# Kernel tuning notes

Measured on AMD Instinct MI355X. Metric: run time of the kernel, lower is better.

The kernel has to match this reference:

```python
import jax, jax.numpy as jnp
import numpy as np

B, L, H, NL = 2048, 32, 512, 64  # batch rows, max children, w_dim, num_labels
EPS = 1e-5


def _layernorm(x, g, b):
    mu = jnp.mean(x, axis=-1, keepdims=True)
    var = jnp.mean((x - mu) ** 2, axis=-1, keepdims=True)
    return (x - mu) * jax.lax.rsqrt(var + EPS) * g + b


def _lstm(x, Wih, Whh, bih, bhh):
    # x: [B, L, D] -> h: [B, L, H]; PyTorch gate order i, f, g, o
    Bs, Ls, _ = x.shape
    Hh = Whh.shape[1]
    xg = jnp.einsum('bld,gd->blg', x, Wih) + bih + bhh  # [B, L, 4H]

    def step(carry, xg_t):
        h, c = carry
        gates = xg_t + h @ Whh.T
        i, f, g, o = jnp.split(gates, 4, axis=-1)
        c = jax.nn.sigmoid(f) * c + jax.nn.sigmoid(i) * jnp.tanh(g)
        h = jax.nn.sigmoid(o) * jnp.tanh(c)
        return (h, c), h

    init = (jnp.zeros((Bs, Hh), x.dtype), jnp.zeros((Bs, Hh), x.dtype))
    _, hs = jax.lax.scan(step, init, jnp.swapaxes(xg, 0, 1))
    return jnp.swapaxes(hs, 0, 1)


def setup_inputs() -> dict:
    key = jax.random.key(0)
    ks = jax.random.split(key, 20)
    n = lambda k, shape, s=0.05: (jax.random.normal(k, shape, jnp.float32) * s)
    return {
        'children': n(ks[0], (B, L, H), 1.0),
        'ch_lengths': jax.random.randint(ks[1], (B,), 1, L + 1),
        'nt': n(ks[2], (B, H), 1.0),
        'nt_id': jax.random.randint(ks[3], (B,), 0, NL),
        'stack_state': n(ks[4], (B, H), 1.0),
        'Wih_f': n(ks[5], (4 * H, H)), 'Whh_f': n(ks[6], (4 * H, H)),
        'bih_f': jnp.zeros(4 * H, jnp.float32), 'bhh_f': jnp.zeros(4 * H, jnp.float32),
        'Wih_b': n(ks[7], (4 * H, H)), 'Whh_b': n(ks[8], (4 * H, H)),
        'bih_b': jnp.zeros(4 * H, jnp.float32), 'bhh_b': jnp.zeros(4 * H, jnp.float32),
        'V': n(ks[9], (2 * H, 2 * H)),
        'nt_emb': n(ks[10], (NL, H), 1.0),
        'nt_emb2': n(ks[11], (NL, 2 * H), 1.0),
        'ln1_g': jnp.ones(2 * H, jnp.float32), 'ln1_b': jnp.zeros(2 * H, jnp.float32),
        'ln2_g': jnp.ones(2 * H, jnp.float32), 'ln2_b': jnp.zeros(2 * H, jnp.float32),
        'gate_W': n(ks[12], (2 * H, 4 * H)), 'gate_b': jnp.zeros(2 * H, jnp.float32),
        'out_W': n(ks[13], (H, 2 * H)), 'out_b': jnp.zeros(H, jnp.float32),
    }


def reference(children, ch_lengths, nt, nt_id, stack_state,
              Wih_f, Whh_f, bih_f, bhh_f, Wih_b, Whh_b, bih_b, bhh_b,
              V, nt_emb, nt_emb2, ln1_g, ln1_b, ln2_g, ln2_b,
              gate_W, gate_b, out_W, out_b):
    t = jnp.arange(L)
    valid = (t[None, :] < ch_lengths[:, None])  # [B, L]
    mask = valid[:, :, None].astype(children.dtype)

    # forward direction (padded positions cannot affect earlier outputs)
    h_f = _lstm(children, Wih_f, Whh_f, bih_f, bhh_f) * mask

    # backward direction: emulate packed sequence by per-row reversal over true length
    rev_idx = jnp.clip(ch_lengths[:, None] - 1 - t[None, :], 0, L - 1)  # [B, L]
    x_rev = jnp.take_along_axis(children, rev_idx[:, :, None], axis=1) * mask
    h_b_rev = _lstm(x_rev, Wih_b, Whh_b, bih_b, bhh_b)
    h_b = jnp.take_along_axis(h_b_rev, rev_idx[:, :, None], axis=1) * mask

    h = jnp.concatenate([h_f, h_b], axis=-1)  # [B, L, 2H]

    rhs = jnp.concatenate([nt_emb[nt_id], stack_state], axis=1)  # [B, 2H]
    logit = jnp.einsum('ble,de,bd->bl', h, V, rhs)  # (V h) . rhs
    logit = jnp.where(valid, logit, -jnp.inf)
    attn = jax.nn.softmax(logit, axis=-1)  # [B, L]

    weighted_child = jnp.einsum('ble,bl->be', h, attn)  # [B, 2H]
    weighted_child = _layernorm(weighted_child, ln2_g, ln2_b)

    nt2 = _layernorm(nt_emb2[nt_id], ln1_g, ln1_b)  # [B, 2H]
    gate_in = jnp.concatenate([nt2, weighted_child], axis=-1)  # [B, 4H]
    g = jax.nn.sigmoid(gate_in @ gate_W.T + gate_b)  # [B, 2H]
    c = g * nt2 + (1.0 - g) * weighted_child
    out = jax.nn.relu(c @ out_W.T + out_b)  # [B, H]
    return (out, attn, g)
```

## Files before the change

kernel.cpp:

```cpp
#include <hip/hip_runtime.h>

#define B_ 2048
#define L_ 32
#define H_ 512
#define H2 1024
#define H4 2048

typedef _Float16 half8 __attribute__((ext_vector_type(8)));
typedef _Float16 half4v __attribute__((ext_vector_type(4)));
typedef float f32x4 __attribute__((ext_vector_type(4)));

__device__ __forceinline__ float sigm(float x) { return 1.f / (1.f + __expf(-x)); }
__device__ __forceinline__ float tanh_f(float x) {
  float ax = fabsf(x);
  float e = __expf(2.f * ax);
  float t = 1.f - 2.f / (e + 1.f);
  return x < 0.f ? -t : t;
}
__device__ __forceinline__ float wave_sum(float v) {
#pragma unroll
  for (int o = 32; o; o >>= 1) v += __shfl_xor(v, o);
  return v;
}

__device__ __forceinline__ void gload_lds16(const _Float16* g, _Float16* l) {
  __builtin_amdgcn_global_load_lds((const __attribute__((address_space(1))) void*)g,
                                   (__attribute__((address_space(3))) void*)l, 16, 0, 0);
}

__global__ __launch_bounds__(256, 2) void gemm_bt(
    const _Float16* __restrict__ A, int lda,
    const _Float16* __restrict__ Bmat, int ldb,
    float* __restrict__ C, int ldc, int K)
{
  __shared__ _Float16 As[2][128 * 64];
  __shared__ _Float16 Bs[2][128 * 64];
  const int tid = threadIdx.x;
  const int lane = tid & 63;
  const int w = tid >> 6;
  const int n0 = blockIdx.x * 128;
  const int m0 = blockIdx.y * 128;

  const int srow = lane >> 3;
  const int kcs = ((lane & 7) ^ srow) << 3;

  f32x4 acc[4][4] = {};
  const int wm = (w >> 1) * 64;
  const int wn = (w & 1) * 64;
  const int fr = lane & 15;

  const int nkt = K >> 6;
  auto stage = [&](int buf, int kt) {
    const int k0 = kt << 6;
#pragma unroll
    for (int i = 0; i < 4; ++i) {
      const int R0 = w * 32 + i * 8;
      gload_lds16(A + (size_t)(m0 + R0 + srow) * lda + (k0 + kcs), &As[buf][R0 * 64]);
      gload_lds16(Bmat + (size_t)(n0 + R0 + srow) * ldb + (k0 + kcs), &Bs[buf][R0 * 64]);
    }
  };

  stage(0, 0);
  __syncthreads();
  int cur = 0;
  for (int kt = 0; kt < nkt; ++kt) {
    if (kt + 1 < nkt) stage(cur ^ 1, kt + 1);
    const char* Ab = (const char*)&As[cur][0];
    const char* Bb = (const char*)&Bs[cur][0];
#pragma unroll
    for (int kk = 0; kk < 2; ++kk) {
      const int so = (((kk << 2) + (lane >> 4)) ^ (fr & 7)) << 4;
      half8 af[4], bf[4];
#pragma unroll
      for (int m = 0; m < 4; ++m) af[m] = *(const half8*)(Ab + (wm + m * 16 + fr) * 128 + so);
#pragma unroll
      for (int n = 0; n < 4; ++n) bf[n] = *(const half8*)(Bb + (wn + n * 16 + fr) * 128 + so);
#pragma unroll
      for (int m = 0; m < 4; ++m)
#pragma unroll
        for (int n = 0; n < 4; ++n)
          acc[m][n] = __builtin_amdgcn_mfma_f32_16x16x32_f16(af[m], bf[n], acc[m][n], 0, 0, 0);
    }
    __syncthreads();
    cur ^= 1;
  }

  const int r0 = (lane >> 4) * 4;
#pragma unroll
  for (int m = 0; m < 4; ++m)
#pragma unroll
    for (int n = 0; n < 4; ++n)
#pragma unroll
      for (int r = 0; r < 4; ++r) {
        const int row = m0 + wm + m * 16 + r0 + r;
        const int col = n0 + wn + n * 16 + fr;
        C[(size_t)row * ldc + col] = acc[m][n][r];
      }
}

__global__ __launch_bounds__(256, 2) void gemm_lstm(
    const _Float16* __restrict__ Wpack,
    const float* __restrict__ bpack,
    const _Float16* __restrict__ chH,
    _Float16* __restrict__ hstate,
    float* __restrict__ cstate,
    _Float16* __restrict__ h_all,
    const int* __restrict__ perm,
    const int* __restrict__ lens_sorted,
    int step)
{
  const int lin = blockIdx.x;
  const int xcd = lin & 7;
  const int g8 = lin >> 3;
  const int dir = xcd >> 2;
  const int quad = xcd & 3;
  const int mt = (quad >> 1) * 8 + (g8 >> 3);
  const int nt = (quad & 1) * 8 + (g8 & 7);
  const int m0 = mt * 128;
  const int n0 = nt * 128;
  if (lens_sorted[m0] <= step) return;

  __shared__ _Float16 As[2][128 * 64];
  __shared__ _Float16 Bs[2][128 * 64];
  const int tid = threadIdx.x;
  const int lane = tid & 63;
  const int w = tid >> 6;

  const int srow = lane >> 3;
  const int kcs = ((lane & 7) ^ srow) << 3;

  const _Float16* xsrc[4];
  int posr[4];
#pragma unroll
  for (int i = 0; i < 4; ++i) {
    const int pos = m0 + w * 32 + i * 8 + srow;
    const int b = perm[pos];
    int idx;
    if (dir == 0) idx = step;
    else { const int t = lens_sorted[pos] - 1 - step; idx = t < 0 ? 0 : (t > 31 ? 31 : t); }
    xsrc[i] = chH + ((size_t)b * L_ + idx) * H_ + kcs;
    posr[i] = pos;
  }
  const _Float16* Wb = Wpack + (size_t)dir * H4 * H2;
  const _Float16* hs = hstate + (size_t)dir * B_ * H_;

  f32x4 acc[4][4] = {};
  const int wm = (w >> 1) * 64;
  const int wn = (w & 1) * 64;
  const int fr = lane & 15;

  auto stage = [&](int buf, int kt) {
    const int k0 = kt << 6;
#pragma unroll
    for (int i = 0; i < 4; ++i) {
      const int R0 = w * 32 + i * 8;
      const _Float16* sA = (k0 < 512) ? (xsrc[i] + k0)
                                      : (hs + (size_t)posr[i] * H_ + (k0 - 512) + kcs);
      gload_lds16(sA, &As[buf][R0 * 64]);
      gload_lds16(Wb + (size_t)(n0 + R0 + srow) * H2 + k0 + kcs, &Bs[buf][R0 * 64]);
    }
  };

  stage(0, 0);
  __syncthreads();
  int cur = 0;
  for (int kt = 0; kt < 16; ++kt) {
    if (kt + 1 < 16) stage(cur ^ 1, kt + 1);
    const char* Ab = (const char*)&As[cur][0];
    const char* Bb = (const char*)&Bs[cur][0];
#pragma unroll
    for (int kk = 0; kk < 2; ++kk) {
      const int so = (((kk << 2) + (lane >> 4)) ^ (fr & 7)) << 4;
      half8 af[4], bf[4];
#pragma unroll
      for (int m = 0; m < 4; ++m) af[m] = *(const half8*)(Ab + (wm + m * 16 + fr) * 128 + so);
#pragma unroll
      for (int n = 0; n < 4; ++n) bf[n] = *(const half8*)(Bb + (wn + n * 16 + fr) * 128 + so);
#pragma unroll
      for (int m = 0; m < 4; ++m)
#pragma unroll
        for (int n = 0; n < 4; ++n)
          acc[m][n] = __builtin_amdgcn_mfma_f32_16x16x32_f16(af[m], bf[n], acc[m][n], 0, 0, 0);
    }
    __syncthreads();
    cur ^= 1;
  }

  const int r0 = (lane >> 4) * 4;
  const int j = ((n0 + wn) >> 6) * 16 + fr;
  const float bi = bpack[dir * H4 + n0 + wn + 0 * 16 + fr];
  const float bf_ = bpack[dir * H4 + n0 + wn + 1 * 16 + fr];
  const float bg = bpack[dir * H4 + n0 + wn + 2 * 16 + fr];
  const float bo = bpack[dir * H4 + n0 + wn + 3 * 16 + fr];
  float* cs = cstate + (size_t)dir * B_ * H_;
  _Float16* hsw = hstate + (size_t)dir * B_ * H_;

#pragma unroll
  for (int m = 0; m < 4; ++m)
#pragma unroll
    for (int r = 0; r < 4; ++r) {
      const int pos = m0 + wm + m * 16 + r0 + r;
      const float zi = acc[m][0][r] + bi;
      const float zf = acc[m][1][r] + bf_;
      const float zg = acc[m][2][r] + bg;
      const float zo = acc[m][3][r] + bo;
      const size_t ci = (size_t)pos * H_ + j;
      const float cn = sigm(zf) * cs[ci] + sigm(zi) * tanh_f(zg);
      const float h = sigm(zo) * tanh_f(cn);
      cs[ci] = cn;
      hsw[ci] = (_Float16)h;
      const int len = lens_sorted[pos];
      if (step < len) {
        const int b = perm[pos];
        const int t = (dir == 0) ? step : (len - 1 - step);
        h_all[((size_t)b * L_ + t) * H2 + dir * 512 + j] = (_Float16)h;
      }
    }
}

__global__ void cast_half_k(const float* __restrict__ s, _Float16* __restrict__ d, int n) {
  const int i = (blockIdx.x * 256 + threadIdx.x) * 4;
  if (i >= n) return;
  const float4 v = *(const float4*)(s + i);
  half4v h;
  h[0] = (_Float16)v.x; h[1] = (_Float16)v.y; h[2] = (_Float16)v.z; h[3] = (_Float16)v.w;
  *(half4v*)(d + i) = h;
}

__global__ void pack_wcat(const float* __restrict__ Wih_f, const float* __restrict__ Whh_f,
                          const float* __restrict__ Wih_b, const float* __restrict__ Whh_b,
                          _Float16* __restrict__ Wcat) {
  const int idx = blockIdx.x * 256 + threadIdx.x;
  const int k = idx & 511;
  const int c = (idx >> 9) & 2047;
  const int dir = idx >> 20;
  const int g = (c >> 4) & 3;
  const int j = ((c >> 6) << 4) + (c & 15);
  const int n_orig = g * 512 + j;
  const float* Wih = dir ? Wih_b : Wih_f;
  const float* Whh = dir ? Whh_b : Whh_f;
  _Float16* row = Wcat + ((size_t)dir * H4 + c) * H2;
  row[k] = (_Float16)Wih[(size_t)n_orig * H_ + k];
  row[512 + k] = (_Float16)Whh[(size_t)n_orig * H_ + k];
}

__global__ void pack_bias(const float* __restrict__ bih_f, const float* __restrict__ bhh_f,
                          const float* __restrict__ bih_b, const float* __restrict__ bhh_b,
                          float* __restrict__ biascat) {
  const int idx = blockIdx.x * 256 + threadIdx.x;
  const int dir = idx >> 11;
  const int c = idx & 2047;
  const int g = (c >> 4) & 3;
  const int j = ((c >> 6) << 4) + (c & 15);
  const int n = g * 512 + j;
  biascat[idx] = dir ? (bih_b[n] + bhh_b[n]) : (bih_f[n] + bhh_f[n]);
}

__global__ void transpose_v(const float* __restrict__ V, _Float16* __restrict__ Vt) {
  const int idx = blockIdx.x * 256 + threadIdx.x;
  const int d = idx >> 10;
  const int e = idx & 1023;
  Vt[(size_t)e * H2 + d] = (_Float16)V[idx];
}

__global__ void build_rhs(const float* __restrict__ nt_emb, const int* __restrict__ nt_id,
                          const float* __restrict__ stack_state, _Float16* __restrict__ rhs_h) {
  const int idx = blockIdx.x * 256 + threadIdx.x;
  const int b = idx >> 10;
  const int d = idx & 1023;
  const float v = (d < 512) ? nt_emb[(size_t)nt_id[b] * H_ + d]
                            : stack_state[(size_t)b * H_ + (d - 512)];
  rhs_h[idx] = (_Float16)v;
}

__global__ void sort1_k(const int* __restrict__ lens, int* __restrict__ offs, int* __restrict__ cursor) {
  __shared__ int cnt[33];
  const int tid = threadIdx.x;
  if (tid < 33) cnt[tid] = 0;
  __syncthreads();
  for (int i = tid; i < B_; i += 256) atomicAdd(&cnt[lens[i]], 1);
  __syncthreads();
  if (tid == 0) {
    int acc = 0;
    for (int l = 32; l >= 1; --l) { offs[l] = acc; acc += cnt[l]; }
  }
  if (tid < 33) cursor[tid] = 0;
}

__global__ void sort2_k(const int* __restrict__ lens, const int* __restrict__ offs,
                        int* __restrict__ cursor, int* __restrict__ perm,
                        int* __restrict__ lens_sorted) {
  const int b = blockIdx.x * 256 + threadIdx.x;
  const int len = lens[b];
  const int pos = offs[len] + atomicAdd(&cursor[len], 1);
  perm[pos] = b;
  lens_sorted[pos] = len;
}

__global__ void marker_k(float* out) { out[threadIdx.x] = 12345.0f; }

__global__ __launch_bounds__(256) void attn_kernel(
    const _Float16* __restrict__ h_all, const float* __restrict__ u,
    const int* __restrict__ lens,
    const float* __restrict__ g2, const float* __restrict__ b2,
    float* __restrict__ attn_out, float* __restrict__ wc_f, _Float16* __restrict__ gin_h) {
  __shared__ float u_s[H2];
  __shared__ float logit_s[L_];
  __shared__ float attn_s[L_];
  __shared__ float red_s[8];
  const int b = blockIdx.x;
  const int tid = threadIdx.x;
  const int lane = tid & 63;
  const int w = tid >> 6;
#pragma unroll
  for (int r = 0; r < 4; ++r) u_s[tid + r * 256] = u[(size_t)b * H2 + tid + r * 256];
  __syncthreads();
  const _Float16* hb = h_all + (size_t)b * L_ * H2;
  const int len = lens[b];
#pragma unroll
  for (int li = 0; li < 8; ++li) {
    const int l = w * 8 + li;
    float p = 0.f;
    if (l < len) {
      const _Float16* hr = hb + (size_t)l * H2;
#pragma unroll
      for (int j = 0; j < 16; ++j) {
        const int e = lane + 64 * j;
        p += (float)hr[e] * u_s[e];
      }
      p = wave_sum(p);
    }
    if (lane == 0) logit_s[l] = p;
  }
  __syncthreads();
  if (w == 0) {
    const int l = lane;
    float v = (l < len) ? logit_s[l] : -1e30f;
    float m = v;
#pragma unroll
    for (int o = 32; o; o >>= 1) m = fmaxf(m, __shfl_xor(m, o));
    const float e = (l < len) ? __expf(v - m) : 0.f;
    float s = e;
#pragma unroll
    for (int o = 32; o; o >>= 1) s += __shfl_xor(s, o);
    const float a = e / s;
    if (l < L_) { attn_s[l] = a; attn_out[(size_t)b * L_ + l] = a; }
  }
  __syncthreads();
  float wcv[4] = {0.f, 0.f, 0.f, 0.f};
  for (int l = 0; l < len; ++l) {
    const float a = attn_s[l];
    const _Float16* hr = hb + (size_t)l * H2;
#pragma unroll
    for (int r = 0; r < 4; ++r) wcv[r] += a * (float)hr[tid + r * 256];
  }
  float s1 = wcv[0] + wcv[1] + wcv[2] + wcv[3];
  float s2 = wcv[0] * wcv[0] + wcv[1] * wcv[1] + wcv[2] * wcv[2] + wcv[3] * wcv[3];
  s1 = wave_sum(s1);
  s2 = wave_sum(s2);
  if (lane == 0) { red_s[w] = s1; red_s[4 + w] = s2; }
  __syncthreads();
  const float S1 = red_s[0] + red_s[1] + red_s[2] + red_s[3];
  const float S2 = red_s[4] + red_s[5] + red_s[6] + red_s[7];
  const float mu = S1 * (1.f / H2);
  const float var = S2 * (1.f / H2) - mu * mu;
  const float rstd = rsqrtf(var + 1e-5f);
#pragma unroll
  for (int r = 0; r < 4; ++r) {
    const int e = tid + r * 256;
    const float y = (wcv[r] - mu) * rstd * g2[e] + b2[e];
    wc_f[(size_t)b * H2 + e] = y;
    gin_h[(size_t)b * H4 + H2 + e] = (_Float16)y;
  }
}

__global__ __launch_bounds__(256) void nt2_kernel(
    const float* __restrict__ nt_emb2, const int* __restrict__ nt_id,
    const float* __restrict__ g1, const float* __restrict__ b1,
    float* __restrict__ nt2_f, _Float16* __restrict__ gin_h) {
  __shared__ float red_s[8];
  const int b = blockIdx.x;
  const int tid = threadIdx.x;
  const int lane = tid & 63;
  const int w = tid >> 6;
  const float* x = nt_emb2 + (size_t)nt_id[b] * H2;
  float v[4];
  float s1 = 0.f, s2 = 0.f;
#pragma unroll
  for (int r = 0; r < 4; ++r) {
    v[r] = x[tid + r * 256];
    s1 += v[r];
    s2 += v[r] * v[r];
  }
  s1 = wave_sum(s1);
  s2 = wave_sum(s2);
  if (lane == 0) { red_s[w] = s1; red_s[4 + w] = s2; }
  __syncthreads();
  const float S1 = red_s[0] + red_s[1] + red_s[2] + red_s[3];
  const float S2 = red_s[4] + red_s[5] + red_s[6] + red_s[7];
  const float mu = S1 * (1.f / H2);
  const float var = S2 * (1.f / H2) - mu * mu;
  const float rstd = rsqrtf(var + 1e-5f);
#pragma unroll
  for (int r = 0; r < 4; ++r) {
    const int e = tid + r * 256;
    const float y = (v[r] - mu) * rstd * g1[e] + b1[e];
    nt2_f[(size_t)b * H2 + e] = y;
    gin_h[(size_t)b * H4 + e] = (_Float16)y;
  }
}

__global__ void gate_epi(const float* __restrict__ gpre, const float* __restrict__ gate_b,
                         const float* __restrict__ nt2_f, const float* __restrict__ wc_f,
                         float* __restrict__ g_out, _Float16* __restrict__ cmix_h) {
  const int idx = blockIdx.x * 256 + threadIdx.x;
  const int j = idx & (H2 - 1);
  const float g = sigm(gpre[idx] + gate_b[j]);
  g_out[idx] = g;
  const float c = g * nt2_f[idx] + (1.f - g) * wc_f[idx];
  cmix_h[idx] = (_Float16)c;
}

__global__ void out_epi(const float* __restrict__ opre, const float* __restrict__ out_b,
                        float* __restrict__ outp) {
  const int idx = blockIdx.x * 256 + threadIdx.x;
  const int j = idx & (H_ - 1);
  const float v = opre[idx] + out_b[j];
  outp[idx] = v > 0.f ? v : 0.f;
}

extern "C" void kernel_launch(void* const* d_in, const int* in_sizes, int n_in,
                              void* d_out, int out_size, void* d_ws, size_t ws_size,
                              hipStream_t stream) {
  const float* children = (const float*)d_in[0];
  const int* lens = (const int*)d_in[1];
  const int* nt_id = (const int*)d_in[3];
  const float* stack_state = (const float*)d_in[4];
  const float* Wih_f = (const float*)d_in[5];
  const float* Whh_f = (const float*)d_in[6];
  const float* bih_f = (const float*)d_in[7];
  const float* bhh_f = (const float*)d_in[8];
  const float* Wih_b = (const float*)d_in[9];
  const float* Whh_b = (const float*)d_in[10];
  const float* bih_b = (const float*)d_in[11];
  const float* bhh_b = (const float*)d_in[12];
  const float* V = (const float*)d_in[13];
  const float* nt_emb = (const float*)d_in[14];
  const float* nt_emb2 = (const float*)d_in[15];
  const float* ln1_g = (const float*)d_in[16];
  const float* ln1_b = (const float*)d_in[17];
  const float* ln2_g = (const float*)d_in[18];
  const float* ln2_b = (const float*)d_in[19];
  const float* gate_W = (const float*)d_in[20];
  const float* gate_b = (const float*)d_in[21];
  const float* out_W = (const float*)d_in[22];
  const float* out_b = (const float*)d_in[23];

  float* out = (float*)d_out;
  float* attn_out = out + (size_t)B_ * H_;
  float* g_out = attn_out + (size_t)B_ * L_;

  char* wsp = (char*)d_ws;
  size_t off = 0;
  auto alloc = [&](size_t bytes) {
    char* p = wsp + off;
    off += (bytes + 255) & ~(size_t)255;
    return p;
  };
  _Float16* ch_h = (_Float16*)alloc((size_t)B_ * L_ * H_ * 2);
  _Float16* h_all = (_Float16*)alloc((size_t)B_ * L_ * H2 * 2);
  _Float16* Wcat = (_Float16*)alloc((size_t)2 * H4 * H2 * 2);
  float* biascat = (float*)alloc((size_t)2 * H4 * 4);
  _Float16* Vt = (_Float16*)alloc((size_t)H2 * H2 * 2);
  _Float16* gateWh = (_Float16*)alloc((size_t)H2 * H4 * 2);
  _Float16* outWh = (_Float16*)alloc((size_t)H_ * H2 * 2);
  _Float16* rhs_h = (_Float16*)alloc((size_t)B_ * H2 * 2);
  float* u_f = (float*)alloc((size_t)B_ * H2 * 4);
  _Float16* hstate = (_Float16*)alloc((size_t)2 * B_ * H_ * 2);
  float* cstate = (float*)alloc((size_t)2 * B_ * H_ * 4);
  float* wc_f = (float*)alloc((size_t)B_ * H2 * 4);
  float* nt2_f = (float*)alloc((size_t)B_ * H2 * 4);
  _Float16* gin_h = (_Float16*)alloc((size_t)B_ * H4 * 2);
  float* gpre_f = (float*)alloc((size_t)B_ * H2 * 4);
  _Float16* cmix_h = (_Float16*)alloc((size_t)B_ * H2 * 2);
  float* opre_f = (float*)alloc((size_t)B_ * H_ * 4);
  int* sort_offs = (int*)alloc(64 * 4);
  int* sort_cursor = (int*)alloc(64 * 4);
  int* perm = (int*)alloc((size_t)B_ * 4);
  int* lens_sorted = (int*)alloc((size_t)B_ * 4);

  if (off > ws_size) {
    marker_k<<<1, 64, 0, stream>>>(out);
    return;
  }

  cast_half_k<<<32768, 256, 0, stream>>>(children, ch_h, B_ * L_ * H_);
  cast_half_k<<<2048, 256, 0, stream>>>(gate_W, gateWh, H2 * H4);
  cast_half_k<<<512, 256, 0, stream>>>(out_W, outWh, H_ * H2);
  pack_wcat<<<8192, 256, 0, stream>>>(Wih_f, Whh_f, Wih_b, Whh_b, Wcat);
  pack_bias<<<16, 256, 0, stream>>>(bih_f, bhh_f, bih_b, bhh_b, biascat);
  transpose_v<<<4096, 256, 0, stream>>>(V, Vt);
  build_rhs<<<8192, 256, 0, stream>>>(nt_emb, nt_id, stack_state, rhs_h);
  hipMemsetAsync(hstate, 0, (size_t)2 * B_ * H_ * 2, stream);
  hipMemsetAsync(cstate, 0, (size_t)2 * B_ * H_ * 4, stream);
  sort1_k<<<1, 256, 0, stream>>>(lens, sort_offs, sort_cursor);
  sort2_k<<<8, 256, 0, stream>>>(lens, sort_offs, sort_cursor, perm, lens_sorted);
  nt2_kernel<<<2048, 256, 0, stream>>>(nt_emb2, nt_id, ln1_g, ln1_b, nt2_f, gin_h);

  gemm_bt<<<dim3(8, 16, 1), 256, 0, stream>>>(rhs_h, H2, Vt, H2, u_f, H2, H2);

  for (int t = 0; t < 32; ++t) {
    gemm_lstm<<<512, 256, 0, stream>>>(
        Wcat, biascat, ch_h, hstate, cstate, h_all, perm, lens_sorted, t);
  }

  attn_kernel<<<2048, 256, 0, stream>>>(h_all, u_f, lens, ln2_g, ln2_b, attn_out, wc_f, gin_h);

  gemm_bt<<<dim3(8, 16, 1), 256, 0, stream>>>(gin_h, H4, gateWh, H4, gpre_f, H2, H4);
  gate_epi<<<8192, 256, 0, stream>>>(gpre_f, gate_b, nt2_f, wc_f, g_out, cmix_h);

  gemm_bt<<<dim3(4, 16, 1), 256, 0, stream>>>(cmix_h, H2, outWh, H2, opre_f, H_, H2);
  out_epi<<<4096, 256, 0, stream>>>(opre_f, out_b, out);
}
```

Measured before the change: 1.169 ms.

## Fuse 32 LSTM step launches into one persistent kernel with grid barrier

```diff
diff --git a/kernel.cpp b/kernel.cpp
--- a/kernel.cpp
+++ b/kernel.cpp
@@ -5,6 +5,7 @@
 #define H_ 512
 #define H2 1024
 #define H4 2048
+#define NBLK 512
 
 typedef _Float16 half8 __attribute__((ext_vector_type(8)));
 typedef _Float16 half4v __attribute__((ext_vector_type(4)));
@@ -98,124 +99,158 @@
       }
 }
 
-__global__ __launch_bounds__(256, 2) void gemm_lstm(
+__global__ __launch_bounds__(256, 2) void lstm_persist(
     const _Float16* __restrict__ Wpack,
     const float* __restrict__ bpack,
     const _Float16* __restrict__ chH,
     _Float16* __restrict__ hstate,
-    float* __restrict__ cstate,
     _Float16* __restrict__ h_all,
     const int* __restrict__ perm,
     const int* __restrict__ lens_sorted,
-    int step)
+    int* __restrict__ bar)
 {
   const int lin = blockIdx.x;
   const int xcd = lin & 7;
   const int g8 = lin >> 3;
   const int dir = xcd >> 2;
   const int quad = xcd & 3;
-  const int mt = (quad >> 1) * 8 + (g8 >> 3);
-  const int nt = (quad & 1) * 8 + (g8 & 7);
+  const int mt = ((g8 >> 3) << 1) + (quad >> 1);
+  const int nt = ((quad & 1) << 3) + (g8 & 7);
   const int m0 = mt * 128;
   const int n0 = nt * 128;
-  if (lens_sorted[m0] <= step) return;
 
   __shared__ _Float16 As[2][128 * 64];
   __shared__ _Float16 Bs[2][128 * 64];
   const int tid = threadIdx.x;
   const int lane = tid & 63;
   const int w = tid >> 6;
-
   const int srow = lane >> 3;
   const int kcs = ((lane & 7) ^ srow) << 3;
-
-  const _Float16* xsrc[4];
-  int posr[4];
-#pragma unroll
-  for (int i = 0; i < 4; ++i) {
-    const int pos = m0 + w * 32 + i * 8 + srow;
-    const int b = perm[pos];
-    int idx;
-    if (dir == 0) idx = step;
-    else { const int t = lens_sorted[pos] - 1 - step; idx = t < 0 ? 0 : (t > 31 ? 31 : t); }
-    xsrc[i] = chH + ((size_t)b * L_ + idx) * H_ + kcs;
-    posr[i] = pos;
-  }
-  const _Float16* Wb = Wpack + (size_t)dir * H4 * H2;
-  const _Float16* hs = hstate + (size_t)dir * B_ * H_;
-
-  f32x4 acc[4][4] = {};
   const int wm = (w >> 1) * 64;
   const int wn = (w & 1) * 64;
   const int fr = lane & 15;
-
-  auto stage = [&](int buf, int kt) {
-    const int k0 = kt << 6;
-#pragma unroll
-    for (int i = 0; i < 4; ++i) {
-      const int R0 = w * 32 + i * 8;
-      const _Float16* sA = (k0 < 512) ? (xsrc[i] + k0)
-                                      : (hs + (size_t)posr[i] * H_ + (k0 - 512) + kcs);
-      gload_lds16(sA, &As[buf][R0 * 64]);
-      gload_lds16(Wb + (size_t)(n0 + R0 + srow) * H2 + k0 + kcs, &Bs[buf][R0 * 64]);
-    }
-  };
-
-  stage(0, 0);
-  __syncthreads();
-  int cur = 0;
-  for (int kt = 0; kt < 16; ++kt) {
-    if (kt + 1 < 16) stage(cur ^ 1, kt + 1);
-    const char* Ab = (const char*)&As[cur][0];
-    const char* Bb = (const char*)&Bs[cur][0];
-#pragma unroll
-    for (int kk = 0; kk < 2; ++kk) {
-      const int so = (((kk << 2) + (lane >> 4)) ^ (fr & 7)) << 4;
-      half8 af[4], bf[4];
-#pragma unroll
-      for (int m = 0; m < 4; ++m) af[m] = *(const half8*)(Ab + (wm + m * 16 + fr) * 128 + so);
-#pragma unroll
-      for (int n = 0; n < 4; ++n) bf[n] = *(const half8*)(Bb + (wn + n * 16 + fr) * 128 + so);
-#pragma unroll
-      for (int m = 0; m < 4; ++m)
-#pragma unroll
-        for (int n = 0; n < 4; ++n)
-          acc[m][n] = __builtin_amdgcn_mfma_f32_16x16x32_f16(af[m], bf[n], acc[m][n], 0, 0, 0);
-    }
-    __syncthreads();
-    cur ^= 1;
-  }
-
   const int r0 = (lane >> 4) * 4;
+
+  int browr[4], lenr[4], posr[4];
+#pragma unroll
+  for (int i = 0; i < 4; ++i) {
+    const int pos = m0 + w * 32 + i * 8 + srow;
+    posr[i] = pos;
+    browr[i] = perm[pos];
+    lenr[i] = lens_sorted[pos];
+  }
+  const _Float16* Wb = Wpack + (size_t)dir * H4 * H2;
+
   const int j = ((n0 + wn) >> 6) * 16 + fr;
   const float bi = bpack[dir * H4 + n0 + wn + 0 * 16 + fr];
   const float bf_ = bpack[dir * H4 + n0 + wn + 1 * 16 + fr];
   const float bg = bpack[dir * H4 + n0 + wn + 2 * 16 + fr];
   const float bo = bpack[dir * H4 + n0 + wn + 3 * 16 + fr];
-  float* cs = cstate + (size_t)dir * B_ * H_;
-  _Float16* hsw = hstate + (size_t)dir * B_ * H_;
-
+  int eposr[16], elenr[16], ebrow[16];
 #pragma unroll
   for (int m = 0; m < 4; ++m)
 #pragma unroll
     for (int r = 0; r < 4; ++r) {
       const int pos = m0 + wm + m * 16 + r0 + r;
-      const float zi = acc[m][0][r] + bi;
-      const float zf = acc[m][1][r] + bf_;
-      const float zg = acc[m][2][r] + bg;
-      const float zo = acc[m][3][r] + bo;
-      const size_t ci = (size_t)pos * H_ + j;
-      const float cn = sigm(zf) * cs[ci] + sigm(zi) * tanh_f(zg);
-      const float h = sigm(zo) * tanh_f(cn);
-      cs[ci] = cn;
-      hsw[ci] = (_Float16)h;
-      const int len = lens_sorted[pos];
-      if (step < len) {
-        const int b = perm[pos];
-        const int t = (dir == 0) ? step : (len - 1 - step);
-        h_all[((size_t)b * L_ + t) * H2 + dir * 512 + j] = (_Float16)h;
+      eposr[m * 4 + r] = pos;
+      elenr[m * 4 + r] = lens_sorted[pos];
+      ebrow[m * 4 + r] = perm[pos];
+    }
+
+  float c_reg[16];
+#pragma unroll
+  for (int q = 0; q < 16; ++q) c_reg[q] = 0.f;
+
+  const int my_len = lens_sorted[m0];
+
+  auto stageA = [&](int buf, int kt, int step, const _Float16* hprev) {
+    const int k0 = kt << 6;
+#pragma unroll
+    for (int i = 0; i < 4; ++i) {
+      const int R0 = w * 32 + i * 8;
+      const _Float16* sA;
+      if (k0 < 512) {
+        int idx;
+        if (dir == 0) idx = step;
+        else { const int t2 = lenr[i] - 1 - step; idx = t2 < 0 ? 0 : (t2 > 31 ? 31 : t2); }
+        sA = chH + ((size_t)browr[i] * L_ + idx) * H_ + k0 + kcs;
+      } else {
+        sA = hprev + (size_t)posr[i] * H_ + (k0 - 512) + kcs;
       }
-    }
+      gload_lds16(sA, &As[buf][R0 * 64]);
+      gload_lds16(Wb + (size_t)(n0 + R0 + srow) * H2 + k0 + kcs, &Bs[buf][R0 * 64]);
+    }
+  };
+
+  stageA(0, 0, 0, nullptr);
+
+  for (int t = 0; t < 32; ++t) {
+    const bool alive = t < my_len;
+    if (alive) {
+      const _Float16* hprev = hstate + ((size_t)((t & 1) * 2 + dir)) * B_ * H_;
+      _Float16* hnext = hstate + ((size_t)(((t + 1) & 1) * 2 + dir)) * B_ * H_;
+
+      f32x4 acc[4][4] = {};
+      __syncthreads();
+      int cur = 0;
+      for (int kt = 0; kt < 16; ++kt) {
+        if (kt + 1 < 16) stageA(cur ^ 1, kt + 1, t, hprev);
+        const char* Ab = (const char*)&As[cur][0];
+        const char* Bb = (const char*)&Bs[cur][0];
+#pragma unroll
+        for (int kk = 0; kk < 2; ++kk) {
+          const int so = (((kk << 2) + (lane >> 4)) ^ (fr & 7)) << 4;
+          half8 af[4], bf[4];
+#pragma unroll
+          for (int m = 0; m < 4; ++m) af[m] = *(const half8*)(Ab + (wm + m * 16 + fr) * 128 + so);
+#pragma unroll
+          for (int n = 0; n < 4; ++n) bf[n] = *(const half8*)(Bb + (wn + n * 16 + fr) * 128 + so);
+#pragma unroll
+          for (int m = 0; m < 4; ++m)
+#pragma unroll
+            for (int n = 0; n < 4; ++n)
+              acc[m][n] = __builtin_amdgcn_mfma_f32_16x16x32_f16(af[m], bf[n], acc[m][n], 0, 0, 0);
+        }
+        __syncthreads();
+        cur ^= 1;
+      }
+
+      if (t + 1 < my_len) stageA(0, 0, t + 1, nullptr);
+
+#pragma unroll
+      for (int m = 0; m < 4; ++m)
+#pragma unroll
+        for (int r = 0; r < 4; ++r) {
+          const int q = m * 4 + r;
+          const float zi = acc[m][0][r] + bi;
+          const float zf = acc[m][1][r] + bf_;
+          const float zg = acc[m][2][r] + bg;
+          const float zo = acc[m][3][r] + bo;
+          const float cn = sigm(zf) * c_reg[q] + sigm(zi) * tanh_f(zg);
+          const float h = sigm(zo) * tanh_f(cn);
+          c_reg[q] = cn;
+          hnext[(size_t)eposr[q] * H_ + j] = (_Float16)h;
+          const int len = elenr[q];
+          if (t < len) {
+            const int tt = (dir == 0) ? t : (len - 1 - t);
+            h_all[((size_t)ebrow[q] * L_ + tt) * H2 + dir * 512 + j] = (_Float16)h;
+          }
+        }
+    }
+
+    if (t != 31) {
+      __threadfence();
+      __syncthreads();
+      if (tid == 0) {
+        __hip_atomic_fetch_add(bar, 1, __ATOMIC_RELAXED, __HIP_MEMORY_SCOPE_AGENT);
+        const int target = NBLK * (t + 1);
+        while (__hip_atomic_load(bar, __ATOMIC_RELAXED, __HIP_MEMORY_SCOPE_AGENT) < target)
+          __builtin_amdgcn_s_sleep(8);
+      }
+      __syncthreads();
+      __threadfence();
+    }
+  }
 }
 
 __global__ void cast_half_k(const float* __restrict__ s, _Float16* __restrict__ d, int n) {
@@ -476,8 +511,7 @@
   _Float16* outWh = (_Float16*)alloc((size_t)H_ * H2 * 2);
   _Float16* rhs_h = (_Float16*)alloc((size_t)B_ * H2 * 2);
   float* u_f = (float*)alloc((size_t)B_ * H2 * 4);
-  _Float16* hstate = (_Float16*)alloc((size_t)2 * B_ * H_ * 2);
-  float* cstate = (float*)alloc((size_t)2 * B_ * H_ * 4);
+  _Float16* hstate = (_Float16*)alloc((size_t)2 * 2 * B_ * H_ * 2);
   float* wc_f = (float*)alloc((size_t)B_ * H2 * 4);
   float* nt2_f = (float*)alloc((size_t)B_ * H2 * 4);
   _Float16* gin_h = (_Float16*)alloc((size_t)B_ * H4 * 2);
@@ -488,6 +522,7 @@
   int* sort_cursor = (int*)alloc(64 * 4);
   int* perm = (int*)alloc((size_t)B_ * 4);
   int* lens_sorted = (int*)alloc((size_t)B_ * 4);
+  int* bar = (int*)alloc(256);
 
   if (off > ws_size) {
     marker_k<<<1, 64, 0, stream>>>(out);
@@ -501,18 +536,16 @@
   pack_bias<<<16, 256, 0, stream>>>(bih_f, bhh_f, bih_b, bhh_b, biascat);
   transpose_v<<<4096, 256, 0, stream>>>(V, Vt);
   build_rhs<<<8192, 256, 0, stream>>>(nt_emb, nt_id, stack_state, rhs_h);
-  hipMemsetAsync(hstate, 0, (size_t)2 * B_ * H_ * 2, stream);
-  hipMemsetAsync(cstate, 0, (size_t)2 * B_ * H_ * 4, stream);
+  hipMemsetAsync(hstate, 0, (size_t)2 * 2 * B_ * H_ * 2, stream);
+  hipMemsetAsync(bar, 0, 256, stream);
   sort1_k<<<1, 256, 0, stream>>>(lens, sort_offs, sort_cursor);
   sort2_k<<<8, 256, 0, stream>>>(lens, sort_offs, sort_cursor, perm, lens_sorted);
   nt2_kernel<<<2048, 256, 0, stream>>>(nt_emb2, nt_id, ln1_g, ln1_b, nt2_f, gin_h);
 
   gemm_bt<<<dim3(8, 16, 1), 256, 0, stream>>>(rhs_h, H2, Vt, H2, u_f, H2, H2);
 
-  for (int t = 0; t < 32; ++t) {
-    gemm_lstm<<<512, 256, 0, stream>>>(
-        Wcat, biascat, ch_h, hstate, cstate, h_all, perm, lens_sorted, t);
-  }
+  lstm_persist<<<NBLK, 256, 0, stream>>>(
+      Wcat, biascat, ch_h, hstate, h_all, perm, lens_sorted, bar);
 
   attn_kernel<<<2048, 256, 0, stream>>>(h_all, u_f, lens, ln2_g, ln2_b, attn_out, wc_f, gin_h);
 
```

New measurement: 4.138 ms. 254% more time.

## Double-buffer LSTM hidden state, use vmcnt waits with raw barriers, remap tiles

Applied to the files above, without the earlier changes.

```diff
diff --git a/kernel.cpp b/kernel.cpp
--- a/kernel.cpp
+++ b/kernel.cpp
@@ -27,6 +27,9 @@
   __builtin_amdgcn_global_load_lds((const __attribute__((address_space(1))) void*)g,
                                    (__attribute__((address_space(3))) void*)l, 16, 0, 0);
 }
+
+__device__ __forceinline__ void wait_vm8() { asm volatile("s_waitcnt vmcnt(8)" ::: "memory"); }
+__device__ __forceinline__ void wait_vm0() { asm volatile("s_waitcnt vmcnt(0)" ::: "memory"); }
 
 __global__ __launch_bounds__(256, 2) void gemm_bt(
     const _Float16* __restrict__ A, int lda,
@@ -59,14 +62,9 @@
       gload_lds16(Bmat + (size_t)(n0 + R0 + srow) * ldb + (k0 + kcs), &Bs[buf][R0 * 64]);
     }
   };
-
-  stage(0, 0);
-  __syncthreads();
-  int cur = 0;
-  for (int kt = 0; kt < nkt; ++kt) {
-    if (kt + 1 < nkt) stage(cur ^ 1, kt + 1);
-    const char* Ab = (const char*)&As[cur][0];
-    const char* Bb = (const char*)&Bs[cur][0];
+  auto compute = [&](int buf) {
+    const char* Ab = (const char*)&As[buf][0];
+    const char* Bb = (const char*)&Bs[buf][0];
 #pragma unroll
     for (int kk = 0; kk < 2; ++kk) {
       const int so = (((kk << 2) + (lane >> 4)) ^ (fr & 7)) << 4;
@@ -81,7 +79,17 @@
         for (int n = 0; n < 4; ++n)
           acc[m][n] = __builtin_amdgcn_mfma_f32_16x16x32_f16(af[m], bf[n], acc[m][n], 0, 0, 0);
     }
-    __syncthreads();
+  };
+
+  stage(0, 0);
+  int cur = 0;
+  for (int kt = 0; kt < nkt; ++kt) {
+    const bool pref = (kt + 1 < nkt);
+    if (pref) { stage(cur ^ 1, kt + 1); wait_vm8(); }
+    else      { wait_vm0(); }
+    __builtin_amdgcn_s_barrier();
+    compute(cur);
+    __builtin_amdgcn_s_barrier();
     cur ^= 1;
   }
 
@@ -114,8 +122,8 @@
   const int g8 = lin >> 3;
   const int dir = xcd >> 2;
   const int quad = xcd & 3;
-  const int mt = (quad >> 1) * 8 + (g8 >> 3);
-  const int nt = (quad & 1) * 8 + (g8 & 7);
+  const int mt = ((g8 >> 3) << 1) + (quad >> 1);
+  const int nt = ((quad & 1) << 3) + (g8 & 7);
   const int m0 = mt * 128;
   const int n0 = nt * 128;
   if (lens_sorted[m0] <= step) return;
@@ -125,9 +133,11 @@
   const int tid = threadIdx.x;
   const int lane = tid & 63;
   const int w = tid >> 6;
-
   const int srow = lane >> 3;
   const int kcs = ((lane & 7) ^ srow) << 3;
+  const int wm = (w >> 1) * 64;
+  const int wn = (w & 1) * 64;
+  const int fr = lane & 15;
 
   const _Float16* xsrc[4];
   int posr[4];
@@ -142,12 +152,10 @@
     posr[i] = pos;
   }
   const _Float16* Wb = Wpack + (size_t)dir * H4 * H2;
-  const _Float16* hs = hstate + (size_t)dir * B_ * H_;
+  const _Float16* hprev = hstate + ((size_t)((step & 1) * 2 + dir)) * B_ * H_;
+  _Float16* hnext = hstate + ((size_t)(((step + 1) & 1) * 2 + dir)) * B_ * H_;
 
   f32x4 acc[4][4] = {};
-  const int wm = (w >> 1) * 64;
-  const int wn = (w & 1) * 64;
-  const int fr = lane & 15;
 
   auto stage = [&](int buf, int kt) {
     const int k0 = kt << 6;
@@ -155,19 +163,14 @@
     for (int i = 0; i < 4; ++i) {
       const int R0 = w * 32 + i * 8;
       const _Float16* sA = (k0 < 512) ? (xsrc[i] + k0)
-                                      : (hs + (size_t)posr[i] * H_ + (k0 - 512) + kcs);
+                                      : (hprev + (size_t)posr[i] * H_ + (k0 - 512) + kcs);
       gload_lds16(sA, &As[buf][R0 * 64]);
       gload_lds16(Wb + (size_t)(n0 + R0 + srow) * H2 + k0 + kcs, &Bs[buf][R0 * 64]);
     }
   };
-
-  stage(0, 0);
-  __syncthreads();
-  int cur = 0;
-  for (int kt = 0; kt < 16; ++kt) {
-    if (kt + 1 < 16) stage(cur ^ 1, kt + 1);
-    const char* Ab = (const char*)&As[cur][0];
-    const char* Bb = (const char*)&Bs[cur][0];
+  auto compute = [&](int buf) {
+    const char* Ab = (const char*)&As[buf][0];
+    const char* Bb = (const char*)&Bs[buf][0];
 #pragma unroll
     for (int kk = 0; kk < 2; ++kk) {
       const int so = (((kk << 2) + (lane >> 4)) ^ (fr & 7)) << 4;
@@ -182,7 +185,17 @@
         for (int n = 0; n < 4; ++n)
           acc[m][n] = __builtin_amdgcn_mfma_f32_16x16x32_f16(af[m], bf[n], acc[m][n], 0, 0, 0);
     }
-    __syncthreads();
+  };
+
+  stage(0, 0);
+  int cur = 0;
+  for (int kt = 0; kt < 16; ++kt) {
+    const bool pref = (kt + 1 < 16);
+    if (pref) { stage(cur ^ 1, kt + 1); wait_vm8(); }
+    else      { wait_vm0(); }
+    __builtin_amdgcn_s_barrier();
+    compute(cur);
+    __builtin_amdgcn_s_barrier();
     cur ^= 1;
   }
 
@@ -193,7 +206,6 @@
   const float bg = bpack[dir * H4 + n0 + wn + 2 * 16 + fr];
   const float bo = bpack[dir * H4 + n0 + wn + 3 * 16 + fr];
   float* cs = cstate + (size_t)dir * B_ * H_;
-  _Float16* hsw = hstate + (size_t)dir * B_ * H_;
 
 #pragma unroll
   for (int m = 0; m < 4; ++m)
@@ -208,7 +220,7 @@
       const float cn = sigm(zf) * cs[ci] + sigm(zi) * tanh_f(zg);
       const float h = sigm(zo) * tanh_f(cn);
       cs[ci] = cn;
-      hsw[ci] = (_Float16)h;
+      hnext[ci] = (_Float16)h;
       const int len = lens_sorted[pos];
       if (step < len) {
         const int b = perm[pos];
@@ -476,7 +488,7 @@
   _Float16* outWh = (_Float16*)alloc((size_t)H_ * H2 * 2);
   _Float16* rhs_h = (_Float16*)alloc((size_t)B_ * H2 * 2);
   float* u_f = (float*)alloc((size_t)B_ * H2 * 4);
-  _Float16* hstate = (_Float16*)alloc((size_t)2 * B_ * H_ * 2);
+  _Float16* hstate = (_Float16*)alloc((size_t)2 * 2 * B_ * H_ * 2);
   float* cstate = (float*)alloc((size_t)2 * B_ * H_ * 4);
   float* wc_f = (float*)alloc((size_t)B_ * H2 * 4);
   float* nt2_f = (float*)alloc((size_t)B_ * H2 * 4);
@@ -501,7 +513,7 @@
   pack_bias<<<16, 256, 0, stream>>>(bih_f, bhh_f, bih_b, bhh_b, biascat);
   transpose_v<<<4096, 256, 0, stream>>>(V, Vt);
   build_rhs<<<8192, 256, 0, stream>>>(nt_emb, nt_id, stack_state, rhs_h);
-  hipMemsetAsync(hstate, 0, (size_t)2 * B_ * H_ * 2, stream);
+  hipMemsetAsync(hstate, 0, (size_t)2 * 2 * B_ * H_ * 2, stream);
   hipMemsetAsync(cstate, 0, (size_t)2 * B_ * H_ * 4, stream);
   sort1_k<<<1, 256, 0, stream>>>(lens, sort_offs, sort_cursor);
   sort2_k<<<8, 256, 0, stream>>>(lens, sort_offs, sort_cursor, perm, lens_sorted);
```

After: 1.092 ms. 1.07x faster.
